# Kernel optimization log

Hardware: AMD Instinct MI355X
Metric: run time of the kernel (lower is better)

The kernel has to match this reference:

```python
import jax, jax.numpy as jnp
import numpy as np

B, N, F, H = 8, 4096, 128, 3  # graphs, nodes (max_types), embedding_size, nhid
ALPHA = 0.2                    # leaky-relu slope from StateNetwork's GAT(..., 0.2, ...)
NEG_INF = -9e15                # masked-softmax fill used by standard GraphAttentionLayer


def setup_inputs() -> dict:
    key = jax.random.key(0)
    ks = jax.random.split(key, 6)
    adj = jax.random.randint(ks[0], (B, N, N), 0, 2, dtype=jnp.int32)
    emb = jax.random.normal(ks[1], (N, F), dtype=jnp.float32)            # state_ent_emb.weight
    W = jax.random.normal(ks[2], (F, H), dtype=jnp.float32) * 0.1        # GAT layer weight
    a = jax.random.normal(ks[3], (2 * H, 1), dtype=jnp.float32) * 0.1    # GAT attention vector
    fc1_w = jax.random.normal(ks[4], (100, N * H), dtype=jnp.float32) * 0.01
    fc1_b = jnp.zeros((100,), dtype=jnp.float32)
    return {"adj": adj, "emb": emb, "W": W, "a": a, "fc1_w": fc1_w, "fc1_b": fc1_b}


def reference(adj, emb, W, a, fc1_w, fc1_b):
    # GAT input x = state_ent_emb.weight is SHARED across graphs, so Wh and the
    # unmasked pairwise scores e are computed once; only the adjacency mask varies.
    Wh = emb @ W                                   # [N, H]
    e_src = Wh @ a[:H]                             # [N, 1]
    e_dst = Wh @ a[H:]                             # [N, 1]
    e = jax.nn.leaky_relu(e_src + e_dst.T, negative_slope=ALPHA)  # [N, N]
    masked = jnp.where(adj > 0, e[None, :, :], NEG_INF)           # [B, N, N]
    attn = jax.nn.softmax(masked, axis=-1)                        # [B, N, N]
    h = jnp.einsum('bij,jh->bih', attn, Wh)                       # [B, N, H]
    h = jax.nn.elu(h)                              # concat=True head -> elu
    out = h.reshape(h.shape[0], -1)                # [B, N*H], per-graph flatten
    return out @ fc1_w.T + fc1_b                   # [B, 100]
```

## Files before the change

kernel.cpp:

```cpp
#include <hip/hip_runtime.h>
#include <hip/hip_bf16.h>
#include <math.h>

#define NNODES 4096
#define FDIM 128
#define HDIM 3
#define BGRAPH 8
#define GAT_ALPHA 0.2f

typedef int v4i __attribute__((ext_vector_type(4)));

__global__ __launch_bounds__(256) void wh_kernel(
    const float* __restrict__ emb, const float* __restrict__ W,
    const float* __restrict__ a,
    float4* __restrict__ tbl, float* __restrict__ esrc) {
    int wid = threadIdx.x >> 6, lane = threadIdx.x & 63;
    int i = blockIdx.x * 4 + wid;
    const float2 ev = *reinterpret_cast<const float2*>(emb + (size_t)i * FDIM + lane * 2);
    int t0 = lane * 2;
    float wh0 = ev.x * W[t0 * 3 + 0] + ev.y * W[(t0 + 1) * 3 + 0];
    float wh1 = ev.x * W[t0 * 3 + 1] + ev.y * W[(t0 + 1) * 3 + 1];
    float wh2 = ev.x * W[t0 * 3 + 2] + ev.y * W[(t0 + 1) * 3 + 2];
    for (int off = 32; off >= 1; off >>= 1) {
        wh0 += __shfl_xor(wh0, off);
        wh1 += __shfl_xor(wh1, off);
        wh2 += __shfl_xor(wh2, off);
    }
    if (lane == 0) {
        float es = wh0 * a[0] + wh1 * a[1] + wh2 * a[2];
        float ed = wh0 * a[3] + wh1 * a[4] + wh2 * a[5];
        tbl[i] = make_float4(wh0, wh1, wh2, ed);
        esrc[i] = es;
    }
}

__global__ __launch_bounds__(512, 4) void attn_kernel(
    const int* __restrict__ adj, const float4* __restrict__ tbl,
    const float* __restrict__ esrc, float* __restrict__ hout) {
    __shared__ float4 ltbl[NNODES];
    __shared__ float4 red[8];
    int tid = threadIdx.x;
    int wid = tid >> 6, lane = tid & 63;

    float s0 = 0.f, s1 = 0.f, s2 = 0.f, mx = -INFINITY;
    for (int k = tid; k < NNODES; k += 512) {
        float4 v = tbl[k];
        ltbl[(k & 3) * 1024 + (k >> 2)] = v;
        s0 += v.x; s1 += v.y; s2 += v.z; mx = fmaxf(mx, v.w);
    }
    for (int off = 32; off >= 1; off >>= 1) {
        s0 += __shfl_xor(s0, off);
        s1 += __shfl_xor(s1, off);
        s2 += __shfl_xor(s2, off);
        mx = fmaxf(mx, __shfl_xor(mx, off));
    }
    if (lane == 0) red[wid] = make_float4(s0, s1, s2, mx);
    __syncthreads();
    if (tid < 8) {
        float4 v = red[tid];
        for (int off = 4; off >= 1; off >>= 1) {
            v.x += __shfl_xor(v.x, off);
            v.y += __shfl_xor(v.y, off);
            v.z += __shfl_xor(v.z, off);
            v.w = fmaxf(v.w, __shfl_xor(v.w, off));
        }
        if (tid == 0) red[0] = v;
    }
    __syncthreads();
    const float4 st = red[0];
    const float dmax = st.w;
    const float L2E = 1.4426950408889634f;

    int gw = blockIdx.x * 8 + wid;
    for (int r = gw; r < BGRAPH * NNODES; r += 4096) {
        int i = r & (NNODES - 1);
        float es = esrc[i];
        float m = es + dmax;
        m = fmaxf(m, GAT_ALPHA * m);
        float bias = -m * L2E;
        const v4i* ap = reinterpret_cast<const v4i*>(adj + (size_t)r * NNODES);

        float s = 0.f, a0 = 0.f, a1 = 0.f, a2 = 0.f;
        #pragma unroll 2
        for (int T = 0; T < 16; ++T) {
            v4i av = __builtin_nontemporal_load(ap + T * 64 + lane);
            int base = T * 64 + lane;
            {
                float4 tv = ltbl[0 * 1024 + base];
                float x = es + tv.w; x = fmaxf(x, GAT_ALPHA * x);
                float w = __builtin_amdgcn_exp2f(x * L2E + bias);
                w = (av.x > 0) ? w : 0.f;
                s += w; a0 += w * tv.x; a1 += w * tv.y; a2 += w * tv.z;
            }
            {
                float4 tv = ltbl[1 * 1024 + base];
                float x = es + tv.w; x = fmaxf(x, GAT_ALPHA * x);
                float w = __builtin_amdgcn_exp2f(x * L2E + bias);
                w = (av.y > 0) ? w : 0.f;
                s += w; a0 += w * tv.x; a1 += w * tv.y; a2 += w * tv.z;
            }
            {
                float4 tv = ltbl[2 * 1024 + base];
                float x = es + tv.w; x = fmaxf(x, GAT_ALPHA * x);
                float w = __builtin_amdgcn_exp2f(x * L2E + bias);
                w = (av.z > 0) ? w : 0.f;
                s += w; a0 += w * tv.x; a1 += w * tv.y; a2 += w * tv.z;
            }
            {
                float4 tv = ltbl[3 * 1024 + base];
                float x = es + tv.w; x = fmaxf(x, GAT_ALPHA * x);
                float w = __builtin_amdgcn_exp2f(x * L2E + bias);
                w = (av.w > 0) ? w : 0.f;
                s += w; a0 += w * tv.x; a1 += w * tv.y; a2 += w * tv.z;
            }
        }
        for (int off = 32; off >= 1; off >>= 1) {
            s  += __shfl_xor(s, off);
            a0 += __shfl_xor(a0, off);
            a1 += __shfl_xor(a1, off);
            a2 += __shfl_xor(a2, off);
        }
        if (lane == 0) {
            float h0, h1, h2;
            if (s > 0.f) {
                h0 = a0 / s; h1 = a1 / s; h2 = a2 / s;
            } else {
                h0 = st.x * (1.f / NNODES);
                h1 = st.y * (1.f / NNODES);
                h2 = st.z * (1.f / NNODES);
            }
            h0 = h0 > 0.f ? h0 : expf(h0) - 1.f;
            h1 = h1 > 0.f ? h1 : expf(h1) - 1.f;
            h2 = h2 > 0.f ? h2 : expf(h2) - 1.f;
            float* hp = hout + (size_t)r * 3;
            hp[0] = h0; hp[1] = h1; hp[2] = h2;
        }
    }
}

__global__ void fc_kernel(const float* __restrict__ h, const float* __restrict__ w,
                          const float* __restrict__ bias, float* __restrict__ out) {
    int bo = blockIdx.x;
    int bg = bo / 100, o = bo % 100;
    const float* hrow = h + (size_t)bg * (NNODES * HDIM);
    const float* wrow = w + (size_t)o * (NNODES * HDIM);
    int tid = threadIdx.x;
    float p = 0.f;
    for (int k = tid; k < NNODES * HDIM; k += 256) p += hrow[k] * wrow[k];
    __shared__ float sh[256];
    sh[tid] = p;
    __syncthreads();
    for (int off = 128; off >= 1; off >>= 1) {
        if (tid < off) sh[tid] += sh[tid + off];
        __syncthreads();
    }
    if (tid == 0) out[bo] = sh[0] + bias[o];
}

extern "C" void kernel_launch(void* const* d_in, const int* in_sizes, int n_in,
                              void* d_out, int out_size, void* d_ws, size_t ws_size,
                              hipStream_t stream) {
    const int*   adj  = (const int*)d_in[0];
    const float* emb  = (const float*)d_in[1];
    const float* W    = (const float*)d_in[2];
    const float* a    = (const float*)d_in[3];
    const float* fc1w = (const float*)d_in[4];
    const float* fc1b = (const float*)d_in[5];
    float* out = (float*)d_out;

    char* ws = (char*)d_ws;
    float4* tbl  = (float4*)ws;
    float*  esrc = (float*)(ws + 65536);
    float*  hout = (float*)(ws + 65536 + 16384);

    wh_kernel<<<NNODES / 4, 256, 0, stream>>>(emb, W, a, tbl, esrc);
    attn_kernel<<<512, 512, 0, stream>>>(adj, tbl, esrc, hout);
    fc_kernel<<<BGRAPH * 100, 256, 0, stream>>>(hout, fc1w, fc1b, out);
}
```

Baseline: 108.5 us.

## Share exp computation across all graphs per row in attention kernel

```diff
diff --git a/kernel.cpp b/kernel.cpp
--- a/kernel.cpp
+++ b/kernel.cpp
@@ -68,62 +68,62 @@
     }
     __syncthreads();
     const float4 st = red[0];
-    const float dmax = st.w;
     const float L2E = 1.4426950408889634f;
 
-    int gw = blockIdx.x * 8 + wid;
-    for (int r = gw; r < BGRAPH * NNODES; r += 4096) {
-        int i = r & (NNODES - 1);
-        float es = esrc[i];
-        float m = es + dmax;
-        m = fmaxf(m, GAT_ALPHA * m);
-        float bias = -m * L2E;
-        const v4i* ap = reinterpret_cast<const v4i*>(adj + (size_t)r * NNODES);
+    int i = blockIdx.x * 8 + wid;
+    float es = esrc[i];
+    float m = es + st.w;
+    m = fmaxf(m, GAT_ALPHA * m);
+    float bias = -m * L2E;
 
-        float s = 0.f, a0 = 0.f, a1 = 0.f, a2 = 0.f;
-        #pragma unroll 2
-        for (int T = 0; T < 16; ++T) {
-            v4i av = __builtin_nontemporal_load(ap + T * 64 + lane);
-            int base = T * 64 + lane;
-            {
-                float4 tv = ltbl[0 * 1024 + base];
-                float x = es + tv.w; x = fmaxf(x, GAT_ALPHA * x);
-                float w = __builtin_amdgcn_exp2f(x * L2E + bias);
-                w = (av.x > 0) ? w : 0.f;
-                s += w; a0 += w * tv.x; a1 += w * tv.y; a2 += w * tv.z;
-            }
-            {
-                float4 tv = ltbl[1 * 1024 + base];
-                float x = es + tv.w; x = fmaxf(x, GAT_ALPHA * x);
-                float w = __builtin_amdgcn_exp2f(x * L2E + bias);
-                w = (av.y > 0) ? w : 0.f;
-                s += w; a0 += w * tv.x; a1 += w * tv.y; a2 += w * tv.z;
-            }
-            {
-                float4 tv = ltbl[2 * 1024 + base];
-                float x = es + tv.w; x = fmaxf(x, GAT_ALPHA * x);
-                float w = __builtin_amdgcn_exp2f(x * L2E + bias);
-                w = (av.z > 0) ? w : 0.f;
-                s += w; a0 += w * tv.x; a1 += w * tv.y; a2 += w * tv.z;
-            }
-            {
-                float4 tv = ltbl[3 * 1024 + base];
-                float x = es + tv.w; x = fmaxf(x, GAT_ALPHA * x);
-                float w = __builtin_amdgcn_exp2f(x * L2E + bias);
-                w = (av.w > 0) ? w : 0.f;
-                s += w; a0 += w * tv.x; a1 += w * tv.y; a2 += w * tv.z;
+    const v4i* ap[BGRAPH];
+    #pragma unroll
+    for (int g = 0; g < BGRAPH; ++g)
+        ap[g] = reinterpret_cast<const v4i*>(adj + ((size_t)g * NNODES + i) * NNODES);
+
+    float sw[BGRAPH], a0[BGRAPH], a1[BGRAPH], a2[BGRAPH];
+    #pragma unroll
+    for (int g = 0; g < BGRAPH; ++g) { sw[g] = 0.f; a0[g] = 0.f; a1[g] = 0.f; a2[g] = 0.f; }
+
+    #pragma unroll 1
+    for (int T = 0; T < 16; ++T) {
+        int base = T * 64 + lane;
+        v4i av[BGRAPH];
+        #pragma unroll
+        for (int g = 0; g < BGRAPH; ++g)
+            av[g] = __builtin_nontemporal_load(ap[g] + base);
+        #pragma unroll
+        for (int c = 0; c < 4; ++c) {
+            float4 tv = ltbl[c * 1024 + base];
+            float t = es + tv.w;
+            float x = fmaxf(t, GAT_ALPHA * t);
+            float w = __builtin_amdgcn_exp2f(x * L2E + bias);
+            #pragma unroll
+            for (int g = 0; g < BGRAPH; ++g) {
+                float wg = (av[g][c] > 0) ? w : 0.f;
+                sw[g] += wg;
+                a0[g] += wg * tv.x;
+                a1[g] += wg * tv.y;
+                a2[g] += wg * tv.z;
             }
         }
+    }
+
+    #pragma unroll
+    for (int g = 0; g < BGRAPH; ++g) {
         for (int off = 32; off >= 1; off >>= 1) {
-            s  += __shfl_xor(s, off);
-            a0 += __shfl_xor(a0, off);
-            a1 += __shfl_xor(a1, off);
-            a2 += __shfl_xor(a2, off);
+            sw[g] += __shfl_xor(sw[g], off);
+            a0[g] += __shfl_xor(a0[g], off);
+            a1[g] += __shfl_xor(a1[g], off);
+            a2[g] += __shfl_xor(a2[g], off);
         }
-        if (lane == 0) {
+    }
+    if (lane == 0) {
+        #pragma unroll
+        for (int g = 0; g < BGRAPH; ++g) {
             float h0, h1, h2;
-            if (s > 0.f) {
-                h0 = a0 / s; h1 = a1 / s; h2 = a2 / s;
+            if (sw[g] > 0.f) {
+                h0 = a0[g] / sw[g]; h1 = a1[g] / sw[g]; h2 = a2[g] / sw[g];
             } else {
                 h0 = st.x * (1.f / NNODES);
                 h1 = st.y * (1.f / NNODES);
@@ -132,7 +132,7 @@
             h0 = h0 > 0.f ? h0 : expf(h0) - 1.f;
             h1 = h1 > 0.f ? h1 : expf(h1) - 1.f;
             h2 = h2 > 0.f ? h2 : expf(h2) - 1.f;
-            float* hp = hout + (size_t)r * 3;
+            float* hp = hout + ((size_t)g * NNODES + i) * 3;
             hp[0] = h0; hp[1] = h1; hp[2] = h2;
         }
     }
```

Measured after the change: 128.1 us. 1.18x slower.
